# Optimization experiments

Hardware: AMD Instinct MI355X
Metric: run time of the kernel (lower is better)

Reference implementation:

```python
import jax, jax.numpy as jnp
import numpy as np

N = 50000          # nodes
E = 800000         # edges (before self-loops)
IN_CH = 128
H1, C1 = 8, 32     # layer-1 heads / channels-per-head (concat -> 256)
H2, C2 = 1, 64     # layer-2 (out_channels=64, heads=1)
NEG_SLOPE = 0.2    # PyG GATConv default LeakyReLU slope for attention


def setup_inputs() -> dict:
    key = jax.random.key(0)
    ks = jax.random.split(key, 10)
    x = jax.random.normal(ks[0], (N, IN_CH), dtype=jnp.float32)
    edge_index = jax.random.randint(ks[1], (2, E), 0, N, dtype=jnp.int64)
    s = 0.05
    W1 = jax.random.normal(ks[2], (IN_CH, H1 * C1), dtype=jnp.float32) * s
    a_src1 = jax.random.normal(ks[3], (H1, C1), dtype=jnp.float32) * s
    a_dst1 = jax.random.normal(ks[4], (H1, C1), dtype=jnp.float32) * s
    b1 = jnp.zeros((H1 * C1,), dtype=jnp.float32)
    W2 = jax.random.normal(ks[5], (H1 * C1, H2 * C2), dtype=jnp.float32) * s
    a_src2 = jax.random.normal(ks[6], (H2, C2), dtype=jnp.float32) * s
    a_dst2 = jax.random.normal(ks[7], (H2, C2), dtype=jnp.float32) * s
    b2 = jnp.zeros((H2 * C2,), dtype=jnp.float32)
    return {"x": x, "edge_index": edge_index,
            "W1": W1, "a_src1": a_src1, "a_dst1": a_dst1, "b1": b1,
            "W2": W2, "a_src2": a_src2, "a_dst2": a_dst2, "b2": b2}


def gat_conv(x, src, dst, W, a_src, a_dst, b, heads, ch):
    """PyG GATConv (eval mode): gather -> LeakyReLU attn -> scatter-softmax -> scatter-add."""
    n = x.shape[0]
    h = (x @ W).reshape(n, heads, ch)                     # [N, H, C]
    alpha_s = jnp.einsum('nhc,hc->nh', h, a_src)          # [N, H]
    alpha_d = jnp.einsum('nhc,hc->nh', h, a_dst)
    e = jax.nn.leaky_relu(alpha_s[src] + alpha_d[dst], NEG_SLOPE)  # [E, H]
    # numerically-stable softmax over edges grouped by destination node
    emax = jax.ops.segment_max(e, dst, num_segments=n)
    e = jnp.exp(e - emax[dst])
    denom = jax.ops.segment_sum(e, dst, num_segments=n)
    alpha = e / denom[dst]                                # [E, H]
    out = jax.ops.segment_sum(h[src] * alpha[:, :, None], dst, num_segments=n)  # [N, H, C]
    return out.reshape(n, heads * ch) + b


def reference(x, edge_index, W1, a_src1, a_dst1, b1, W2, a_src2, a_dst2, b2):
    # PyG GATConv adds self-loops by default
    loops = jnp.arange(N, dtype=edge_index.dtype)
    src = jnp.concatenate([edge_index[0], loops])
    dst = jnp.concatenate([edge_index[1], loops])
    h = jax.nn.relu(gat_conv(x, src, dst, W1, a_src1, a_dst1, b1, H1, C1))
    out = jax.nn.relu(gat_conv(h, src, dst, W2, a_src2, a_dst2, b2, H2, C2))
    return out
```

## Files before the change

### kernel.cpp

```cpp
#include <hip/hip_runtime.h>
#include <math.h>

#define NEG_SLOPE 0.2f
__device__ __forceinline__ float leaky(float x) { return fmaxf(x, NEG_SLOPE * x); }

typedef _Float16 f16;
typedef _Float16 f16x4 __attribute__((ext_vector_type(4)));
typedef _Float16 f16x8 __attribute__((ext_vector_type(8)));
typedef float f32x4 __attribute__((ext_vector_type(4)));

__device__ __forceinline__ int kmap(int lh, int e) {
  return (e < 4) ? lh * 4 + e : 16 + lh * 4 + (e - 4);
}

__global__ void k_count(const int* __restrict__ dst, int* __restrict__ deg, int E) {
  int e = blockIdx.x * blockDim.x + threadIdx.x;
  if (e < E) atomicAdd(&deg[dst[e]], 1);
}

#define W1_TOT (17 * 4 * 64 * 8)
#define W2_TOT (5 * 8 * 64 * 8)
__global__ __launch_bounds__(256) void k_partial_packw(const int* __restrict__ deg,
    int* __restrict__ part, int n, int nb,
    const float* __restrict__ W1, const float* __restrict__ as1f,
    const float* __restrict__ ad1f, const float* __restrict__ W2,
    const float* __restrict__ as2f, const float* __restrict__ ad2f,
    f16* __restrict__ Wp1, f16* __restrict__ Wp2) {
  if ((int)blockIdx.x < nb) {
    __shared__ int s[256];
    int i = blockIdx.x * 256 + threadIdx.x;
    s[threadIdx.x] = (i < n) ? deg[i] : 0;
    __syncthreads();
    for (int off = 128; off > 0; off >>= 1) {
      if (threadIdx.x < off) s[threadIdx.x] += s[threadIdx.x + off];
      __syncthreads();
    }
    if (threadIdx.x == 0) part[blockIdx.x] = s[0];
  }
  int tid = blockIdx.x * 256 + threadIdx.x;
  if (tid < W1_TOT) {
    int e = tid & 7, l = (tid >> 3) & 63, ks = (tid >> 9) & 3, nt = tid >> 11;
    int lh = l >> 4, li = l & 15;
    int k = ks * 32 + kmap(lh, e);
    float v;
    if (nt < 16) {
      v = W1[k * 256 + nt * 16 + li];
    } else {
      int h = li & 7;
      const float* a = (li < 8) ? (as1f + h * 32) : (ad1f + h * 32);
      v = 0.f;
      for (int j = 0; j < 32; ++j) v += W1[k * 256 + h * 32 + j] * a[j];
    }
    Wp1[tid] = (f16)v;
  } else if (tid < W1_TOT + W2_TOT) {
    int t2 = tid - W1_TOT;
    int e = t2 & 7, l = (t2 >> 3) & 63, ks = (t2 >> 9) & 7, nt = t2 >> 12;
    int lh = l >> 4, li = l & 15;
    int k = ks * 32 + kmap(lh, e);
    float v = 0.f;
    if (nt < 4) {
      v = W2[k * 64 + nt * 16 + li];
    } else if (li == 0) {
      for (int j = 0; j < 64; ++j) v += W2[k * 64 + j] * as2f[j];
    } else if (li == 1) {
      for (int j = 0; j < 64; ++j) v += W2[k * 64 + j] * ad2f[j];
    }
    Wp2[t2] = (f16)v;
  }
}

__global__ __launch_bounds__(256) void k_offs(int* __restrict__ deg,
                                              const int* __restrict__ part,
                                              int* __restrict__ offs, int n, int nb) {
  __shared__ int ps[256];
  __shared__ int s[256];
  int t = threadIdx.x;
  ps[t] = (t < nb) ? part[t] : 0;
  __syncthreads();
  for (int off = 1; off < 256; off <<= 1) {
    int u = (t >= off) ? ps[t - off] : 0;
    __syncthreads();
    ps[t] += u;
    __syncthreads();
  }
  int base = (blockIdx.x > 0) ? ps[blockIdx.x - 1] : 0;

  int i = blockIdx.x * 256 + t;
  int v = (i < n) ? deg[i] : 0;
  s[t] = v;
  __syncthreads();
  for (int off = 1; off < 256; off <<= 1) {
    int u = (t >= off) ? s[t - off] : 0;
    __syncthreads();
    s[t] += u;
    __syncthreads();
  }
  int excl = base + s[t] - v;
  if (i < n) {
    offs[i] = excl;
    deg[i] = 0;
  }
  if (i == n - 1) offs[n] = excl + v;
}

__global__ __launch_bounds__(256) void k_fill_gemm1(
    const int* __restrict__ src, const int* __restrict__ dst,
    const int* __restrict__ offs, int* __restrict__ cursor,
    int* __restrict__ col, int E, int fillBlocks,
    const float* __restrict__ x, const f16* __restrict__ Wp1,
    f16* __restrict__ h16, float* __restrict__ as, float* __restrict__ ad,
    int n, int nSlots) {
  if ((int)blockIdx.x < fillBlocks) {
    int e = blockIdx.x * 256 + threadIdx.x;
    if (e >= E) return;
    int d = dst[e];
    int pos = atomicAdd(&cursor[d], 1);
    col[offs[d] + pos] = src[e];
    return;
  }
  int slot = (blockIdx.x - fillBlocks) * 4 + (threadIdx.x >> 6);
  if (slot >= nSlots) return;
  int half = slot & 1;
  int wid = slot >> 1;
  int lane = threadIdx.x & 63, lh = lane >> 4, li = lane & 15;
  size_t arow = (size_t)min(wid * 16 + li, n - 1);
  f16x8 a[4];
#pragma unroll
  for (int ks = 0; ks < 4; ++ks) {
    float4 lo = *(const float4*)&x[arow * 128 + ks * 32 + lh * 4];
    float4 hi = *(const float4*)&x[arow * 128 + ks * 32 + 16 + lh * 4];
    a[ks][0] = (f16)lo.x; a[ks][1] = (f16)lo.y; a[ks][2] = (f16)lo.z; a[ks][3] = (f16)lo.w;
    a[ks][4] = (f16)hi.x; a[ks][5] = (f16)hi.y; a[ks][6] = (f16)hi.z; a[ks][7] = (f16)hi.w;
  }
  int rbase = wid * 16 + lh * 4;
  int ntBeg = half ? 8 : 0;
  int ntEnd = half ? 17 : 8;
  for (int nt = ntBeg; nt < ntEnd; ++nt) {
    f32x4 acc = {0.f, 0.f, 0.f, 0.f};
#pragma unroll
    for (int ks = 0; ks < 4; ++ks) {
      f16x8 b = *(const f16x8*)&Wp1[((nt * 4 + ks) * 64 + lane) * 8];
      acc = __builtin_amdgcn_mfma_f32_16x16x32_f16(a[ks], b, acc, 0, 0, 0);
    }
    if (nt < 16) {
#pragma unroll
      for (int r = 0; r < 4; ++r) {
        int rr = rbase + r;
        if (rr < n) h16[(size_t)rr * 256 + nt * 16 + li] = (f16)acc[r];
      }
    } else {
#pragma unroll
      for (int r = 0; r < 4; ++r) {
        int rr = rbase + r;
        if (rr < n) {
          if (li < 8) as[(size_t)rr * 8 + li] = acc[r];
          else        ad[(size_t)rr * 8 + (li - 8)] = acc[r];
        }
      }
    }
  }
}

#define RPAD 264
__global__ __launch_bounds__(256) void k_agg1_gemm2(const f16* __restrict__ h16,
    const float* __restrict__ as, const float* __restrict__ ad,
    const int* __restrict__ offs, const int* __restrict__ col,
    const float* __restrict__ b, const f16* __restrict__ Wp2,
    f16* __restrict__ h2, float* __restrict__ as2, float* __restrict__ ad2, int n) {
  __shared__ f16 rs[16][RPAD];
  int wave = threadIdx.x >> 6;
  int lane = threadIdx.x & 63;
  int head = lane >> 3;
  int c0 = lane * 4;

  for (int i = 0; i < 4; ++i) {
    int rl = wave * 4 + i;
    int node = blockIdx.x * 16 + rl;
    if (node >= n) {
      f16x4 z = {(f16)0.f, (f16)0.f, (f16)0.f, (f16)0.f};
      *(f16x4*)&rs[rl][c0] = z;
      continue;
    }
    node = __builtin_amdgcn_readfirstlane(node);
    int beg = offs[node], end = offs[node + 1];
    float adn = ad[node * 8 + head];

    float denom, ax, ay, az, aw;
    {
      float w = __expf(leaky(as[node * 8 + head] + adn));
      f16x4 g = *(const f16x4*)&h16[(size_t)node * 256 + c0];
      denom = w;
      ax = w * (float)g[0]; ay = w * (float)g[1];
      az = w * (float)g[2]; aw = w * (float)g[3];
    }
    int p = beg;
    for (; p + 8 <= end; p += 8) {
      int s[8];
#pragma unroll
      for (int j = 0; j < 8; ++j) s[j] = col[p + j];
      float e[8];
#pragma unroll
      for (int j = 0; j < 8; ++j) e[j] = as[s[j] * 8 + head];
      f16x4 g[8];
#pragma unroll
      for (int j = 0; j < 8; ++j) g[j] = *(const f16x4*)&h16[(size_t)s[j] * 256 + c0];
      float w[8];
#pragma unroll
      for (int j = 0; j < 8; ++j) w[j] = __expf(leaky(e[j] + adn));
#pragma unroll
      for (int j = 0; j < 8; ++j) {
        denom += w[j];
        ax += w[j] * (float)g[j][0]; ay += w[j] * (float)g[j][1];
        az += w[j] * (float)g[j][2]; aw += w[j] * (float)g[j][3];
      }
    }
    for (; p < end; ++p) {
      int s = col[p];
      float w = __expf(leaky(as[s * 8 + head] + adn));
      f16x4 g = *(const f16x4*)&h16[(size_t)s * 256 + c0];
      denom += w;
      ax += w * (float)g[0]; ay += w * (float)g[1];
      az += w * (float)g[2]; aw += w * (float)g[3];
    }
    float inv = 1.f / denom;
    float4 bv = *(const float4*)&b[c0];
    f16x4 o;
    o[0] = (f16)fmaxf(fmaf(ax, inv, bv.x), 0.f);
    o[1] = (f16)fmaxf(fmaf(ay, inv, bv.y), 0.f);
    o[2] = (f16)fmaxf(fmaf(az, inv, bv.z), 0.f);
    o[3] = (f16)fmaxf(fmaf(aw, inv, bv.w), 0.f);
    *(f16x4*)&rs[rl][c0] = o;
  }
  __syncthreads();

  int lh = lane >> 4, li = lane & 15;
  f16x8 a[8];
#pragma unroll
  for (int ks = 0; ks < 8; ++ks) {
    f16x4 lo = *(const f16x4*)&rs[li][ks * 32 + lh * 4];
    f16x4 hi = *(const f16x4*)&rs[li][ks * 32 + 16 + lh * 4];
    a[ks][0] = lo[0]; a[ks][1] = lo[1]; a[ks][2] = lo[2]; a[ks][3] = lo[3];
    a[ks][4] = hi[0]; a[ks][5] = hi[1]; a[ks][6] = hi[2]; a[ks][7] = hi[3];
  }
  int rbase = blockIdx.x * 16 + lh * 4;
  for (int nt = wave; nt < 5; nt += 4) {
    f32x4 acc = {0.f, 0.f, 0.f, 0.f};
#pragma unroll
    for (int ks = 0; ks < 8; ++ks) {
      f16x8 bb = *(const f16x8*)&Wp2[((nt * 8 + ks) * 64 + lane) * 8];
      acc = __builtin_amdgcn_mfma_f32_16x16x32_f16(a[ks], bb, acc, 0, 0, 0);
    }
    if (nt < 4) {
#pragma unroll
      for (int r = 0; r < 4; ++r) {
        int rr = rbase + r;
        if (rr < n) h2[(size_t)rr * 64 + nt * 16 + li] = (f16)acc[r];
      }
    } else {
#pragma unroll
      for (int r = 0; r < 4; ++r) {
        int rr = rbase + r;
        if (rr < n) {
          if (li == 0) as2[rr] = acc[r];
          else if (li == 1) ad2[rr] = acc[r];
        }
      }
    }
  }
}

__global__ __launch_bounds__(256) void k_agg2(const f16* __restrict__ h2,
    const float* __restrict__ as, const float* __restrict__ ad,
    const int* __restrict__ offs, const int* __restrict__ col,
    const float* __restrict__ b, float* __restrict__ out, int n) {
  int node = blockIdx.x * 4 + (threadIdx.x >> 6);
  if (node >= n) return;
  node = __builtin_amdgcn_readfirstlane(node);
  int lane = threadIdx.x & 63;
  int es = lane >> 4;
  int c = lane & 15;
  int beg = offs[node], end = offs[node + 1];
  int deg = end - beg;
  float adn = ad[node];

  float a0 = 0.f, a1 = 0.f, a2 = 0.f, a3 = 0.f, wsum = 0.f;
  if (es == 0) {
    float w = __expf(leaky(as[node] + adn));
    f16x4 g = *(const f16x4*)&h2[(size_t)node * 64 + c * 4];
    wsum = w;
    a0 = w * (float)g[0]; a1 = w * (float)g[1];
    a2 = w * (float)g[2]; a3 = w * (float)g[3];
  }
  for (int base = 0; base < deg; base += 16) {
    int s[4]; float e[4]; f16x4 g[4]; float w[4];
#pragma unroll
    for (int q = 0; q < 4; ++q) {
      int idx = base + q * 4 + es;
      s[q] = (idx < deg) ? col[beg + idx] : node;
    }
#pragma unroll
    for (int q = 0; q < 4; ++q) e[q] = as[s[q]];
#pragma unroll
    for (int q = 0; q < 4; ++q) g[q] = *(const f16x4*)&h2[(size_t)s[q] * 64 + c * 4];
#pragma unroll
    for (int q = 0; q < 4; ++q) {
      int idx = base + q * 4 + es;
      w[q] = (idx < deg) ? __expf(leaky(e[q] + adn)) : 0.f;
    }
#pragma unroll
    for (int q = 0; q < 4; ++q) {
      wsum += w[q];
      a0 += w[q] * (float)g[q][0]; a1 += w[q] * (float)g[q][1];
      a2 += w[q] * (float)g[q][2]; a3 += w[q] * (float)g[q][3];
    }
  }
  a0 += __shfl_xor(a0, 16, 64); a1 += __shfl_xor(a1, 16, 64);
  a2 += __shfl_xor(a2, 16, 64); a3 += __shfl_xor(a3, 16, 64);
  wsum += __shfl_xor(wsum, 16, 64);
  a0 += __shfl_xor(a0, 32, 64); a1 += __shfl_xor(a1, 32, 64);
  a2 += __shfl_xor(a2, 32, 64); a3 += __shfl_xor(a3, 32, 64);
  wsum += __shfl_xor(wsum, 32, 64);
  if (es == 0) {
    float inv = 1.f / wsum;
    float4 bv = *(const float4*)&b[c * 4];
    f32x4 o;
    o[0] = fmaxf(fmaf(a0, inv, bv.x), 0.f);
    o[1] = fmaxf(fmaf(a1, inv, bv.y), 0.f);
    o[2] = fmaxf(fmaf(a2, inv, bv.z), 0.f);
    o[3] = fmaxf(fmaf(a3, inv, bv.w), 0.f);
    __builtin_nontemporal_store(o, (f32x4*)&out[(size_t)node * 64 + c * 4]);
  }
}

extern "C" void kernel_launch(void* const* d_in, const int* in_sizes, int n_in,
                              void* d_out, int out_size, void* d_ws, size_t ws_size,
                              hipStream_t stream) {
  const float* x      = (const float*)d_in[0];
  const int*   ei     = (const int*)d_in[1];
  const float* W1     = (const float*)d_in[2];
  const float* a_src1 = (const float*)d_in[3];
  const float* a_dst1 = (const float*)d_in[4];
  const float* b1     = (const float*)d_in[5];
  const float* W2     = (const float*)d_in[6];
  const float* a_src2 = (const float*)d_in[7];
  const float* a_dst2 = (const float*)d_in[8];
  const float* b2     = (const float*)d_in[9];

  int N = in_sizes[0] / 128;
  int E = in_sizes[1] / 2;
  const int* srcI = ei;
  const int* dstI = ei + E;
  int nb = (N + 255) / 256;
  int packBlocks = (W1_TOT + W2_TOT + 255) / 256;
  int ppBlocks = nb > packBlocks ? nb : packBlocks;
  int nWaves = (N + 15) / 16;
  int nSlots1 = nWaves * 2;
  int fillBlocks = (E + 255) / 256;
  int gemm1Blocks = (nSlots1 + 3) / 4;
  int nodeBlocks = (N + 3) / 4;
  int aggBlocks = (N + 15) / 16;

  char* ws = (char*)d_ws;
  size_t o = 0;
  auto alloc = [&](size_t bytes) -> void* {
    void* p = ws + o;
    o += (bytes + 255) & ~(size_t)255;
    return p;
  };
  f16*   h1f    = (f16*)alloc((size_t)N * 256 * 2);
  f16*   h2f    = (f16*)alloc((size_t)N * 64 * 2);
  f16*   Wp1    = (f16*)alloc((size_t)W1_TOT * 2);
  f16*   Wp2    = (f16*)alloc((size_t)W2_TOT * 2);
  float* as1    = (float*)alloc((size_t)N * 8 * 4);
  float* ad1    = (float*)alloc((size_t)N * 8 * 4);
  float* as2    = (float*)alloc((size_t)N * 4);
  float* ad2    = (float*)alloc((size_t)N * 4);
  int*   offs   = (int*)alloc((size_t)(N + 1) * 4);
  int*   cursor = (int*)alloc((size_t)N * 4);
  int*   col    = (int*)alloc((size_t)E * 4);
  int*   part   = (int*)alloc((size_t)nb * 4);

  hipMemsetAsync(cursor, 0, (size_t)N * 4, stream);
  k_count<<<(E + 255) / 256, 256, 0, stream>>>(dstI, cursor, E);
  k_partial_packw<<<ppBlocks, 256, 0, stream>>>(cursor, part, N, nb,
      W1, a_src1, a_dst1, W2, a_src2, a_dst2, Wp1, Wp2);
  k_offs<<<nb, 256, 0, stream>>>(cursor, part, offs, N, nb);

  k_fill_gemm1<<<fillBlocks + gemm1Blocks, 256, 0, stream>>>(
      srcI, dstI, offs, cursor, col, E, fillBlocks,
      x, Wp1, h1f, as1, ad1, N, nSlots1);

  k_agg1_gemm2<<<aggBlocks, 256, 0, stream>>>(h1f, as1, ad1, offs, col, b1,
                                              Wp2, h2f, as2, ad2, N);

  k_agg2<<<nodeBlocks, 256, 0, stream>>>(h2f, as2, ad2, offs, col, b2, (float*)d_out, N);
}
```

Before: 210.8 us.

## Record edge rank during counting and balance agg rows via shared work queue

The count kernel now stores the atomicAdd return value as a per-edge rank, so the CSR fill writes col[offs[d]+rank[e]] with no second atomic pass and no cursor reset. The layer-1 aggregation kernel replaces the static four-rows-per-wave assignment with a shared-memory counter that waves pull rows from dynamically, to even out imbalance from varying node degrees. This adds an E-sized rank buffer (extra global writes and reads) and a shared atomic per row.

```diff
diff --git a/kernel.cpp b/kernel.cpp
--- a/kernel.cpp
+++ b/kernel.cpp
@@ -13,9 +13,13 @@
   return (e < 4) ? lh * 4 + e : 16 + lh * 4 + (e - 4);
 }
 
-__global__ void k_count(const int* __restrict__ dst, int* __restrict__ deg, int E) {
+__global__ void k_count(const int* __restrict__ dst, int* __restrict__ deg,
+                        int* __restrict__ rank, int E) {
   int e = blockIdx.x * blockDim.x + threadIdx.x;
-  if (e < E) atomicAdd(&deg[dst[e]], 1);
+  if (e < E) {
+    int d = dst[e];
+    rank[e] = atomicAdd(&deg[d], 1);
+  }
 }
 
 #define W1_TOT (17 * 4 * 64 * 8)
@@ -69,7 +73,7 @@
   }
 }
 
-__global__ __launch_bounds__(256) void k_offs(int* __restrict__ deg,
+__global__ __launch_bounds__(256) void k_offs(const int* __restrict__ deg,
                                               const int* __restrict__ part,
                                               int* __restrict__ offs, int n, int nb) {
   __shared__ int ps[256];
@@ -96,16 +100,13 @@
     __syncthreads();
   }
   int excl = base + s[t] - v;
-  if (i < n) {
-    offs[i] = excl;
-    deg[i] = 0;
-  }
+  if (i < n) offs[i] = excl;
   if (i == n - 1) offs[n] = excl + v;
 }
 
 __global__ __launch_bounds__(256) void k_fill_gemm1(
     const int* __restrict__ src, const int* __restrict__ dst,
-    const int* __restrict__ offs, int* __restrict__ cursor,
+    const int* __restrict__ offs, const int* __restrict__ rank,
     int* __restrict__ col, int E, int fillBlocks,
     const float* __restrict__ x, const f16* __restrict__ Wp1,
     f16* __restrict__ h16, float* __restrict__ as, float* __restrict__ ad,
@@ -114,8 +115,7 @@
     int e = blockIdx.x * 256 + threadIdx.x;
     if (e >= E) return;
     int d = dst[e];
-    int pos = atomicAdd(&cursor[d], 1);
-    col[offs[d] + pos] = src[e];
+    col[offs[d] + rank[e]] = src[e];
     return;
   }
   int slot = (blockIdx.x - fillBlocks) * 4 + (threadIdx.x >> 6);
@@ -168,13 +168,19 @@
     const float* __restrict__ b, const f16* __restrict__ Wp2,
     f16* __restrict__ h2, float* __restrict__ as2, float* __restrict__ ad2, int n) {
   __shared__ f16 rs[16][RPAD];
+  __shared__ int nextNode;
   int wave = threadIdx.x >> 6;
   int lane = threadIdx.x & 63;
   int head = lane >> 3;
   int c0 = lane * 4;
-
-  for (int i = 0; i < 4; ++i) {
-    int rl = wave * 4 + i;
+  if (threadIdx.x == 0) nextNode = 0;
+  __syncthreads();
+
+  for (;;) {
+    int rl = 0;
+    if (lane == 0) rl = atomicAdd(&nextNode, 1);
+    rl = __shfl(rl, 0, 64);
+    if (rl >= 16) break;
     int node = blockIdx.x * 16 + rl;
     if (node >= n) {
       f16x4 z = {(f16)0.f, (f16)0.f, (f16)0.f, (f16)0.f};
@@ -376,18 +382,19 @@
   float* as2    = (float*)alloc((size_t)N * 4);
   float* ad2    = (float*)alloc((size_t)N * 4);
   int*   offs   = (int*)alloc((size_t)(N + 1) * 4);
-  int*   cursor = (int*)alloc((size_t)N * 4);
+  int*   deg    = (int*)alloc((size_t)N * 4);
+  int*   rank   = (int*)alloc((size_t)E * 4);
   int*   col    = (int*)alloc((size_t)E * 4);
   int*   part   = (int*)alloc((size_t)nb * 4);
 
-  hipMemsetAsync(cursor, 0, (size_t)N * 4, stream);
-  k_count<<<(E + 255) / 256, 256, 0, stream>>>(dstI, cursor, E);
-  k_partial_packw<<<ppBlocks, 256, 0, stream>>>(cursor, part, N, nb,
+  hipMemsetAsync(deg, 0, (size_t)N * 4, stream);
+  k_count<<<(E + 255) / 256, 256, 0, stream>>>(dstI, deg, rank, E);
+  k_partial_packw<<<ppBlocks, 256, 0, stream>>>(deg, part, N, nb,
       W1, a_src1, a_dst1, W2, a_src2, a_dst2, Wp1, Wp2);
-  k_offs<<<nb, 256, 0, stream>>>(cursor, part, offs, N, nb);
+  k_offs<<<nb, 256, 0, stream>>>(deg, part, offs, N, nb);
 
   k_fill_gemm1<<<fillBlocks + gemm1Blocks, 256, 0, stream>>>(
-      srcI, dstI, offs, cursor, col, E, fillBlocks,
+      srcI, dstI, offs, rank, col, E, fillBlocks,
       x, Wp1, h1f, as1, ad1, N, nSlots1);
 
   k_agg1_gemm2<<<aggBlocks, 256, 0, stream>>>(h1f, as1, ad1, offs, col, b1,
```

Measured after the change: 185.1 us. 12.2% less time.
